# Performance work log

Hardware: AMD Instinct MI355X
Metric: run time of the kernel (lower is better)

Reference implementation:

```python
import jax, jax.numpy as jnp
import numpy as np

LOG_2PI = float(np.log(2.0 * np.pi))


def setup_inputs() -> dict:
    key = jax.random.key(0)
    k1, k2, k3 = jax.random.split(key, 3)
    B, T, F, K = 16, 1024, 1024, 500
    X = jax.random.normal(k1, (B, T, F), dtype=jnp.float32)
    mu = jax.random.normal(k2, (K, F), dtype=jnp.float32)
    # cov must be positive for log(cov); uniform in [0.5, 1.5)
    cov = jax.random.uniform(k3, (K, F), dtype=jnp.float32) + 0.5
    return {"X": X, "mu": mu, "cov": cov}


def reference(X, mu, cov):
    # Diagonal-covariance GMM log-likelihoods: out[b,t,k] = log N(X[b,t]; mu[k], diag(cov[k]))
    # Algebraic expansion of 0.5*sum((x-mu)^2/cov) into two GEMMs + bias, avoiding
    # the BxTxKxF broadcast intermediate. Same math as the torch module.
    D = mu.shape[-1]
    inv_cov = 1.0 / cov                                   # (K, F)
    C = -0.5 * D * LOG_2PI - 0.5 * jnp.sum(jnp.log(cov), axis=-1)  # (K,)
    quad = jnp.einsum('btf,kf->btk', X * X, inv_cov)      # sum x^2/cov
    cross = jnp.einsum('btf,kf->btk', X, mu * inv_cov)    # sum x*mu/cov
    const = jnp.sum(mu * mu * inv_cov, axis=-1)           # (K,) sum mu^2/cov
    ULL = 0.5 * (quad - 2.0 * cross + const[None, None, :])
    return C[None, None, :] - ULL                         # (B, T, K)
```

## Files before the change

### kernel.cpp

```cpp
#include <hip/hip_runtime.h>
#include <hip/hip_bf16.h>


typedef __attribute__((ext_vector_type(8))) __bf16 bf16x8;
typedef __attribute__((ext_vector_type(4))) float  f32x4;

#define LOG_2PI 1.837877066409345339082f

constexpr int M_TOT = 16384;
constexpr int F_DIM = 1024;
constexpr int K_GMM = 500;
constexpr int N_PAD = 512;

constexpr int BM  = 128;
constexpr int BN  = 128;
constexpr int BKF = 32;
constexpr int NIT = F_DIM / BKF;

__device__ __forceinline__ unsigned pack_sq_x(float x) {
    __hip_bfloat162 h = __float22bfloat162_rn(make_float2(x * x, x));
    union { __hip_bfloat162 h; unsigned u; } cv;
    cv.h = h;
    return cv.u;
}

__global__ __launch_bounds__(256) void prep_w_kernel(
    const float* __restrict__ mu, const float* __restrict__ cov,
    unsigned* __restrict__ Wimg, float* __restrict__ bias)
{
    const int k = blockIdx.x;
    const int t = threadIdx.x;
    const int tt  = k >> 7;
    const int wch = (k >> 6) & 1;
    const int b   = (k >> 4) & 3;
    const int lo  = k & 15;
    float sl = 0.f, sq = 0.f;
    #pragma unroll
    for (int j = 0; j < 4; ++j) {
        const int d  = t + j * 256;
        const int it = d >> 5;
        const int c  = (d >> 4) & 1;
        const int hi = (d >> 2) & 3;
        const int jj = d & 3;
        const int dw = ((((tt * 2 + wch) * 32 + it) * 8) + (b * 2 + c)) * 256
                     + (hi * 16 + lo) * 4 + jj;
        if (k < K_GMM) {
            const float cv_ = cov[k * F_DIM + d];
            const float m_  = mu[k * F_DIM + d];
            const float ic  = 1.0f / cv_;
            __hip_bfloat162 h = __float22bfloat162_rn(make_float2(-0.5f * ic, m_ * ic));
            union { __hip_bfloat162 h; unsigned u; } cvt; cvt.h = h;
            Wimg[dw] = cvt.u;
            sl += logf(cv_);
            sq += m_ * m_ * ic;
        } else {
            Wimg[dw] = 0u;
        }
    }
    #pragma unroll
    for (int off = 32; off > 0; off >>= 1) {
        sl += __shfl_down(sl, off, 64);
        sq += __shfl_down(sq, off, 64);
    }
    __shared__ float red[8];
    if ((t & 63) == 0) { red[(t >> 6) * 2] = sl; red[(t >> 6) * 2 + 1] = sq; }
    __syncthreads();
    if (t == 0) {
        const float SL = red[0] + red[2] + red[4] + red[6];
        const float SQ = red[1] + red[3] + red[5] + red[7];
        bias[k] = (k < K_GMM)
                ? (-0.5f * (F_DIM * LOG_2PI) - 0.5f * SL - 0.5f * SQ) : 0.f;
    }
}

__global__ __launch_bounds__(512, 4) void gemm_kernel(
    const float* __restrict__ X, const unsigned* __restrict__ Wimg,
    const float* __restrict__ bias, float* __restrict__ out)
{
    __shared__ __align__(16) char smem[32768];
    float* ep = reinterpret_cast<float*>(smem);

    const int bid    = blockIdx.x;
    const int m_base = (bid & 127) * BM;
    const int n_tile = bid >> 7;
    const int n_base = n_tile * BN;

    const int tid  = threadIdx.x;
    const int lane = tid & 63;
    const int wv   = tid >> 6;
    const int wr   = (wv >> 1) * 32;
    const int wch  = wv & 1;
    const int wc   = wch * 64;
    const int hi   = lane >> 4;
    const int lo   = lane & 15;
    const int lsw  = lo & 7;

    const int sr = tid >> 2;
    const int sc = tid & 3;

    const float4* Xv = reinterpret_cast<const float4*>(X);
    const bf16x8* Wf = reinterpret_cast<const bf16x8*>(Wimg);
    const int wbase = (n_tile * 2 + wch) * 32 * 8 * 64;

    f32x4 acc[2][4];
    #pragma unroll
    for (int a = 0; a < 2; ++a)
        #pragma unroll
        for (int b = 0; b < 4; ++b)
            acc[a][b] = (f32x4){0.f, 0.f, 0.f, 0.f};

    auto loadA = [&](int itS, float4* ar) {
        #pragma unroll
        for (int j = 0; j < 2; ++j)
            ar[j] = Xv[(size_t)(m_base + sr) * (F_DIM / 4) + itS * 8 + sc * 2 + j];
    };
    auto packA = [&](const float4* ar, int ab) {
        unsigned short* Ad = reinterpret_cast<unsigned short*>(smem + ab * 16384);
        #pragma unroll
        for (int j = 0; j < 2; ++j) {
            const int chunk = (sc * 2 + j) ^ (sr & 7);
            uint4 wa;
            wa.x = pack_sq_x(ar[j].x);
            wa.y = pack_sq_x(ar[j].y);
            wa.z = pack_sq_x(ar[j].z);
            wa.w = pack_sq_x(ar[j].w);
            *reinterpret_cast<uint4*>(&Ad[sr * 64 + chunk * 8]) = wa;
        }
    };
    auto loadB = [&](int itS, bf16x8* br) {
        #pragma unroll
        for (int f = 0; f < 8; ++f)
            br[f] = Wf[wbase + (itS * 8 + f) * 64 + lane];
    };
    auto mfmas = [&](int ab, const bf16x8* br) {
        const unsigned short* Asc =
            reinterpret_cast<const unsigned short*>(smem + ab * 16384);
        #pragma unroll
        for (int c = 0; c < 2; ++c) {
            bf16x8 af[2];
            #pragma unroll
            for (int a = 0; a < 2; ++a) {
                const int row   = wr + a * 16 + lo;
                const int chunk = (c * 4 + hi) ^ lsw;
                af[a] = *reinterpret_cast<const bf16x8*>(&Asc[row * 64 + chunk * 8]);
            }
            __builtin_amdgcn_s_setprio(1);
            #pragma unroll
            for (int a = 0; a < 2; ++a)
                #pragma unroll
                for (int b = 0; b < 4; ++b)
                    acc[a][b] = __builtin_amdgcn_mfma_f32_16x16x32_bf16(
                        af[a], br[b * 2 + c], acc[a][b], 0, 0, 0);
            __builtin_amdgcn_s_setprio(0);
        }
    };

    float4 aA[2];
    bf16x8 bb[8];
    loadA(0, aA);
    loadB(0, bb);
    packA(aA, 0);
    loadA(1, aA);
    asm volatile("s_waitcnt lgkmcnt(0)" ::: "memory");
    __builtin_amdgcn_s_barrier();
    __builtin_amdgcn_sched_barrier(0);

    for (int it = 0; it < NIT; ++it) {
        const int ab = it & 1;
        if (it + 1 < NIT) {
            packA(aA, ab ^ 1);
            if (it + 2 < NIT) loadA(it + 2, aA);
        }
        mfmas(ab, bb);
        if (it + 1 < NIT) loadB(it + 1, bb);
        asm volatile("s_waitcnt lgkmcnt(0)" ::: "memory");
        __builtin_amdgcn_s_barrier();
        __builtin_amdgcn_sched_barrier(0);
    }

    const int ncols = (K_GMM - n_base < BN) ? (K_GMM - n_base) : BN;
    #pragma unroll
    for (int p = 0; p < 2; ++p) {
        if (p) __syncthreads();
        if ((wv >> 2) == p) {
            #pragma unroll
            for (int b = 0; b < 4; ++b) {
                const int col = wc + b * 16 + lo;
                const float bv = bias[n_base + col];
                const int er0 = ((wv >> 1) & 1) * 32;
                #pragma unroll
                for (int a = 0; a < 2; ++a) {
                    const int er = er0 + a * 16 + hi * 4;
                    #pragma unroll
                    for (int i = 0; i < 4; ++i)
                        ep[(er + i) * 128 + col] = acc[a][b][i] + bv;
                }
            }
        }
        __syncthreads();
        #pragma unroll
        for (int q = 0; q < 4; ++q) {
            const int f    = q * 512 + tid;
            const int row  = f >> 5;
            const int slot = f & 31;
            if (slot * 4 < ncols) {
                const float4 v = *reinterpret_cast<const float4*>(&ep[row * 128 + slot * 4]);
                *reinterpret_cast<float4*>(
                    &out[(size_t)(m_base + p * 64 + row) * K_GMM + n_base + slot * 4]) = v;
            }
        }
    }
}

extern "C" void kernel_launch(void* const* d_in, const int* in_sizes, int n_in,
                              void* d_out, int out_size, void* d_ws, size_t ws_size,
                              hipStream_t stream)
{
    (void)in_sizes; (void)n_in; (void)out_size; (void)ws_size;
    const float* X   = (const float*)d_in[0];
    const float* mu  = (const float*)d_in[1];
    const float* cov = (const float*)d_in[2];
    float* out = (float*)d_out;

    unsigned* Wimg = (unsigned*)d_ws;
    float*    bias = (float*)((char*)d_ws + (size_t)N_PAD * F_DIM * 4);

    prep_w_kernel<<<dim3(N_PAD), dim3(256), 0, stream>>>(mu, cov, Wimg, bias);
    gemm_kernel<<<dim3((M_TOT / BM) * (N_PAD / BN)), dim3(512), 0, stream>>>(X, Wimg, bias, out);
}
```

Before: 59.69 us.

## Split K dimension across two wave groups with shared-memory reduction

The 8 waves are split into two groups that each cover half of the F reduction dimension (16 iterations instead of 32). Each wave now owns a 64x64 output tile with 16 accumulators, which doubles register pressure. Partial sums from group 1 are staged in a 64 KB LDS buffer and added by group 0 before the store. The aim is to halve the serial k-loop and increase per-wave MFMA reuse of A and B fragments. The cost is lower occupancy from the extra LDS and registers, plus an extra reduction pass.

```diff
diff --git a/kernel.cpp b/kernel.cpp
--- a/kernel.cpp
+++ b/kernel.cpp
@@ -15,7 +15,7 @@
 constexpr int BM  = 128;
 constexpr int BN  = 128;
 constexpr int BKF = 32;
-constexpr int NIT = F_DIM / BKF;
+constexpr int NIT = 16;
 
 __device__ __forceinline__ unsigned pack_sq_x(float x) {
     __hip_bfloat162 h = __float22bfloat162_rn(make_float2(x * x, x));
@@ -77,7 +77,7 @@
     const float* __restrict__ X, const unsigned* __restrict__ Wimg,
     const float* __restrict__ bias, float* __restrict__ out)
 {
-    __shared__ __align__(16) char smem[32768];
+    __shared__ __align__(16) char smem[65536];
     float* ep = reinterpret_cast<float*>(smem);
 
     const int bid    = blockIdx.x;
@@ -88,37 +88,43 @@
     const int tid  = threadIdx.x;
     const int lane = tid & 63;
     const int wv   = tid >> 6;
-    const int wr   = (wv >> 1) * 32;
-    const int wch  = wv & 1;
+    const int grp  = wv >> 2;
+    const int gw   = wv & 3;
+    const int wr   = (gw >> 1) * 64;
+    const int wch  = gw & 1;
     const int wc   = wch * 64;
     const int hi   = lane >> 4;
     const int lo   = lane & 15;
     const int lsw  = lo & 7;
-
-    const int sr = tid >> 2;
-    const int sc = tid & 3;
+    const int kbase = grp * 16;
+
+    const int gtid = tid & 255;
+    const int sr   = gtid >> 1;
+    const int sh   = gtid & 1;
 
     const float4* Xv = reinterpret_cast<const float4*>(X);
     const bf16x8* Wf = reinterpret_cast<const bf16x8*>(Wimg);
     const int wbase = (n_tile * 2 + wch) * 32 * 8 * 64;
 
-    f32x4 acc[2][4];
-    #pragma unroll
-    for (int a = 0; a < 2; ++a)
+    f32x4 acc[4][4];
+    #pragma unroll
+    for (int a = 0; a < 4; ++a)
         #pragma unroll
         for (int b = 0; b < 4; ++b)
             acc[a][b] = (f32x4){0.f, 0.f, 0.f, 0.f};
 
     auto loadA = [&](int itS, float4* ar) {
         #pragma unroll
-        for (int j = 0; j < 2; ++j)
-            ar[j] = Xv[(size_t)(m_base + sr) * (F_DIM / 4) + itS * 8 + sc * 2 + j];
+        for (int j = 0; j < 4; ++j)
+            ar[j] = Xv[(size_t)(m_base + sr) * (F_DIM / 4)
+                       + (kbase + itS) * 8 + sh * 4 + j];
     };
     auto packA = [&](const float4* ar, int ab) {
-        unsigned short* Ad = reinterpret_cast<unsigned short*>(smem + ab * 16384);
-        #pragma unroll
-        for (int j = 0; j < 2; ++j) {
-            const int chunk = (sc * 2 + j) ^ (sr & 7);
+        unsigned short* Ad =
+            reinterpret_cast<unsigned short*>(smem + grp * 32768 + ab * 16384);
+        #pragma unroll
+        for (int j = 0; j < 4; ++j) {
+            const int chunk = (sh * 4 + j) ^ (sr & 7);
             uint4 wa;
             wa.x = pack_sq_x(ar[j].x);
             wa.y = pack_sq_x(ar[j].y);
@@ -130,23 +136,23 @@
     auto loadB = [&](int itS, bf16x8* br) {
         #pragma unroll
         for (int f = 0; f < 8; ++f)
-            br[f] = Wf[wbase + (itS * 8 + f) * 64 + lane];
+            br[f] = Wf[wbase + ((kbase + itS) * 8 + f) * 64 + lane];
     };
     auto mfmas = [&](int ab, const bf16x8* br) {
         const unsigned short* Asc =
-            reinterpret_cast<const unsigned short*>(smem + ab * 16384);
+            reinterpret_cast<const unsigned short*>(smem + grp * 32768 + ab * 16384);
         #pragma unroll
         for (int c = 0; c < 2; ++c) {
-            bf16x8 af[2];
-            #pragma unroll
-            for (int a = 0; a < 2; ++a) {
+            bf16x8 af[4];
+            #pragma unroll
+            for (int a = 0; a < 4; ++a) {
                 const int row   = wr + a * 16 + lo;
                 const int chunk = (c * 4 + hi) ^ lsw;
                 af[a] = *reinterpret_cast<const bf16x8*>(&Asc[row * 64 + chunk * 8]);
             }
             __builtin_amdgcn_s_setprio(1);
             #pragma unroll
-            for (int a = 0; a < 2; ++a)
+            for (int a = 0; a < 4; ++a)
                 #pragma unroll
                 for (int b = 0; b < 4; ++b)
                     acc[a][b] = __builtin_amdgcn_mfma_f32_16x16x32_bf16(
@@ -155,7 +161,7 @@
         }
     };
 
-    float4 aA[2];
+    float4 aA[4];
     bf16x8 bb[8];
     loadA(0, aA);
     loadB(0, bb);
@@ -178,36 +184,46 @@
         __builtin_amdgcn_sched_barrier(0);
     }
 
+    if (grp == 1) {
+        #pragma unroll
+        for (int b = 0; b < 4; ++b) {
+            const int col = wc + b * 16 + lo;
+            #pragma unroll
+            for (int a = 0; a < 4; ++a) {
+                const int er = wr + a * 16 + hi * 4;
+                #pragma unroll
+                for (int i = 0; i < 4; ++i)
+                    ep[(er + i) * 128 + col] = acc[a][b][i];
+            }
+        }
+    }
+    __syncthreads();
+    if (grp == 0) {
+        #pragma unroll
+        for (int b = 0; b < 4; ++b) {
+            const int col = wc + b * 16 + lo;
+            const float bv = bias[n_base + col];
+            #pragma unroll
+            for (int a = 0; a < 4; ++a) {
+                const int er = wr + a * 16 + hi * 4;
+                #pragma unroll
+                for (int i = 0; i < 4; ++i)
+                    ep[(er + i) * 128 + col] += acc[a][b][i] + bv;
+            }
+        }
+    }
+    __syncthreads();
+
     const int ncols = (K_GMM - n_base < BN) ? (K_GMM - n_base) : BN;
     #pragma unroll
-    for (int p = 0; p < 2; ++p) {
-        if (p) __syncthreads();
-        if ((wv >> 2) == p) {
-            #pragma unroll
-            for (int b = 0; b < 4; ++b) {
-                const int col = wc + b * 16 + lo;
-                const float bv = bias[n_base + col];
-                const int er0 = ((wv >> 1) & 1) * 32;
-                #pragma unroll
-                for (int a = 0; a < 2; ++a) {
-                    const int er = er0 + a * 16 + hi * 4;
-                    #pragma unroll
-                    for (int i = 0; i < 4; ++i)
-                        ep[(er + i) * 128 + col] = acc[a][b][i] + bv;
-                }
-            }
-        }
-        __syncthreads();
-        #pragma unroll
-        for (int q = 0; q < 4; ++q) {
-            const int f    = q * 512 + tid;
-            const int row  = f >> 5;
-            const int slot = f & 31;
-            if (slot * 4 < ncols) {
-                const float4 v = *reinterpret_cast<const float4*>(&ep[row * 128 + slot * 4]);
-                *reinterpret_cast<float4*>(
-                    &out[(size_t)(m_base + p * 64 + row) * K_GMM + n_base + slot * 4]) = v;
-            }
+    for (int q = 0; q < 8; ++q) {
+        const int f    = q * 512 + tid;
+        const int row  = f >> 5;
+        const int slot = f & 31;
+        if (slot * 4 < ncols) {
+            const float4 v = *reinterpret_cast<const float4*>(&ep[row * 128 + slot * 4]);
+            *reinterpret_cast<float4*>(
+                &out[(size_t)(m_base + row) * K_GMM + n_base + slot * 4]) = v;
         }
     }
 }
```

New measurement: 101.5 us. +70.0%, slower.
